# Kernel optimization log

Measured on AMD Instinct MI355X. Metric: run time of the kernel, lower is better.

## Reference

```python
import jax, jax.numpy as jnp
import numpy as np

NUM_FILTER = 256
CAPS_LEN = 8
NUM_EMOTIONS = 8
OUT_DIM = 16
NUM_CHANNEL = 25
TIME_LEN = 25
NUM_CAPS = NUM_CHANNEL * TIME_LEN * (NUM_FILTER // CAPS_LEN)  # 20000
NUM_ITERATIONS = 3


def setup_inputs() -> dict:
    key = jax.random.key(0)
    ks = jax.random.split(key, 10)
    B = 32
    x = jax.random.normal(ks[0], (B, 54, 54), jnp.float32)
    conv1_w = jax.random.normal(ks[1], (NUM_FILTER, 1, 6, 6), jnp.float32) * 0.05
    conv1_b = jax.random.normal(ks[2], (NUM_FILTER,), jnp.float32) * 0.01
    conv2_w = jax.random.normal(ks[3], (NUM_FILTER, NUM_FILTER, 6, 6), jnp.float32) * 0.01
    conv2_b = jax.random.normal(ks[4], (NUM_FILTER,), jnp.float32) * 0.01
    conv3_w = jax.random.normal(ks[5], (NUM_FILTER, 2 * NUM_FILTER, 1, 1), jnp.float32) * 0.05
    conv3_b = jax.random.normal(ks[6], (NUM_FILTER,), jnp.float32) * 0.01
    # PrimaryCaps: one Linear(caps_len -> caps_len) per capsule, batched as [nc, out, in]
    pc_w = jax.random.normal(ks[7], (NUM_CAPS, CAPS_LEN, CAPS_LEN), jnp.float32) * 0.1
    pc_b = jax.random.normal(ks[8], (NUM_CAPS, CAPS_LEN), jnp.float32) * 0.1
    # EmotionCaps transform W: [nc, num_emotions, out_dim, in_dim]
    W = jax.random.normal(ks[9], (NUM_CAPS, NUM_EMOTIONS, OUT_DIM, CAPS_LEN), jnp.float32) * 0.05
    return {"x": x, "conv1_w": conv1_w, "conv1_b": conv1_b, "conv2_w": conv2_w,
            "conv2_b": conv2_b, "conv3_w": conv3_w, "conv3_b": conv3_b,
            "pc_w": pc_w, "pc_b": pc_b, "W": W}


def _conv(x, w, b, stride):
    y = jax.lax.conv_general_dilated(x, w, (stride, stride), 'VALID',
                                     dimension_numbers=('NCHW', 'OIHW', 'NCHW'))
    return y + b[None, :, None, None]


def _squash(s):
    # scale = |s|^2 / (1 + |s|^2); out = scale * s / (|s| + 1e-8)
    n2 = jnp.sum(s * s, axis=-1, keepdims=True)
    n = jnp.sqrt(n2)
    return (n2 / (1.0 + n2)) * s / (n + 1e-8)


def reference(x, conv1_w, conv1_b, conv2_w, conv2_b, conv3_w, conv3_b, pc_w, pc_b, W):
    x4 = x[:, None]                                    # [B,1,54,54]
    x1 = jax.nn.relu(_conv(x4, conv1_w, conv1_b, 2))   # [B,F,25,25]
    y = jnp.pad(x1, ((0, 0), (0, 0), (2, 3), (2, 3)))  # ZeroPad2d((2,3,2,3))
    y = jax.nn.relu(_conv(y, conv2_w, conv2_b, 1))     # [B,F,25,25]
    z = jax.nn.relu(jnp.concatenate([x1, y], axis=1))  # [B,2F,25,25]
    z = _conv(z, conv3_w, conv3_b, 1)                  # [B,F,25,25]
    B, F, H, Wd = z.shape
    # flatten to capsules: [B, F//caps_len, caps_len, H*W] -> [B, nc, caps_len]
    caps = z.reshape(B, F // CAPS_LEN, CAPS_LEN, H * Wd)
    caps = caps.transpose(0, 1, 3, 2).reshape(B, NUM_CAPS, CAPS_LEN)
    # PrimaryCaps: per-capsule linear, batched as a single einsum
    u = jnp.einsum('bni,noi->bno', caps, pc_w) + pc_b[None]   # [B,nc,caps_len]
    # EmotionCaps: u_hat[b,n,e,o] = W[n,e,o,i] u[b,n,i]
    u_hat = jnp.einsum('bni,neoi->bneo', u, W)                # [B,nc,ne,out_dim]
    b = jnp.zeros((B, NUM_CAPS, NUM_EMOTIONS), u.dtype)
    v = None
    for r in range(NUM_ITERATIONS):
        c = jax.nn.softmax(b, axis=2)[..., None]              # [B,nc,ne,1]
        v = _squash(jnp.sum(c * u_hat, axis=1))               # [B,ne,out_dim]
        if r < NUM_ITERATIONS - 1:
            b = b + jnp.einsum('bneo,beo->bne', u_hat, v)
    return jnp.linalg.norm(v, axis=-1)                        # [B,ne]
```

## Files before the change

kernel.cpp:

```cpp
#include <hip/hip_runtime.h>
#include <hip/hip_fp16.h>

typedef unsigned short u16;
typedef __attribute__((ext_vector_type(8))) short bf16x8;
typedef __attribute__((ext_vector_type(4))) float floatx4;
typedef __attribute__((ext_vector_type(2))) _Float16 half2v;

#define NPIX 625
#define NCAPS 20000
#define K2 9216

__device__ __forceinline__ u16 f2bf(float f) {
  unsigned u = __float_as_uint(f);
  return (u16)((u + 0x7fffu + ((u >> 16) & 1u)) >> 16);
}

__device__ __forceinline__ unsigned h16(float f) {
  union { _Float16 h; u16 b; } c;
  c.h = (_Float16)f;
  return (unsigned)c.b;
}

__device__ __forceinline__ half2v as_h2(unsigned u) {
  union { unsigned i; half2v h; } c;
  c.i = u;
  return c.h;
}

__device__ __forceinline__ float dot2f(unsigned a, unsigned b, float c) {
#if __has_builtin(__builtin_amdgcn_fdot2)
  return __builtin_amdgcn_fdot2(as_h2(a), as_h2(b), c, false);
#else
  half2v x = as_h2(a), y = as_h2(b);
  return fmaf((float)x[1], (float)y[1], fmaf((float)x[0], (float)y[0], c));
#endif
}

__device__ __forceinline__ float dotrow16(uint4 w, uint4 u) {
  float s = dot2f(w.x, u.x, 0.f);
  s = dot2f(w.y, u.y, s);
  s = dot2f(w.z, u.z, s);
  s = dot2f(w.w, u.w, s);
  return s;
}

__device__ __forceinline__ float dot8v(float4 a0, float4 a1, float4 b0, float4 b1) {
  float s = a0.x * b0.x;
  s = fmaf(a0.y, b0.y, s); s = fmaf(a0.z, b0.z, s); s = fmaf(a0.w, b0.w, s);
  s = fmaf(a1.x, b1.x, s); s = fmaf(a1.y, b1.y, s);
  s = fmaf(a1.z, b1.z, s); s = fmaf(a1.w, b1.w, s);
  return s;
}

#define GLDS16(g, l) __builtin_amdgcn_global_load_lds( \
    (const __attribute__((address_space(1))) void*)(g), \
    (__attribute__((address_space(3))) void*)(l), 16, 0, 0)

__global__ void prep_conv1(const float* __restrict__ w2, const float* __restrict__ w3,
                           u16* __restrict__ A2c, u16* __restrict__ A3,
                           const float* __restrict__ x, const float* __restrict__ w1,
                           const float* __restrict__ b1, u16* __restrict__ x1p) {
  if (blockIdx.x < 256) {
    const int oc = blockIdx.x, c = threadIdx.x;
    const float* src = w2 + (oc * 256 + c) * 36;
    float v[36];
#pragma unroll
    for (int k = 0; k < 9; k++) {
      const float4 q = *(const float4*)(src + k * 4);
      v[k * 4 + 0] = q.x; v[k * 4 + 1] = q.y; v[k * 4 + 2] = q.z; v[k * 4 + 3] = q.w;
    }
    const int mtile = oc >> 7, row = oc & 127;
#pragma unroll
    for (int t = 0; t < 36; t++) {
      const int kt = t / 9, tl = t % 9;
      A2c[(kt * 2 + mtile) * 294912 + row * 2304 + tl * 256 + c] = f2bf(v[t]);
    }
  } else if (blockIdx.x < 384) {
    const int j = (blockIdx.x - 256) * 1024 + threadIdx.x * 4;
    const float4 q = *(const float4*)(w3 + j);
    ushort4 p;
    p.x = f2bf(q.x); p.y = f2bf(q.y); p.z = f2bf(q.z); p.w = f2bf(q.w);
    *(ushort4*)(A3 + j) = p;
  } else {
    const int blk = blockIdx.x - 384;
    const int b = blk / 25, i = blk % 25;
    const int f = threadIdx.x;
    float wreg[36];
#pragma unroll
    for (int k = 0; k < 36; k++) wreg[k] = w1[f * 36 + k];
    float bias = b1[f];
    const float* xb = x + b * 54 * 54 + (2 * i) * 54;
    for (int j = 0; j < 25; j++) {
      float acc = bias;
#pragma unroll
      for (int ki = 0; ki < 6; ki++)
#pragma unroll
        for (int kj = 0; kj < 6; kj++)
          acc = fmaf(xb[ki * 54 + 2 * j + kj], wreg[ki * 6 + kj], acc);
      x1p[(((b * 30 + i + 2) * 30) + (j + 2)) * 256 + f] = f2bf(fmaxf(acc, 0.f));
    }
  }
}

__global__ __launch_bounds__(256) void conv2_gemm(const u16* __restrict__ A2c,
    const u16* __restrict__ x1p, u16* __restrict__ P) {
  __shared__ u16 As0[128 * 32];
  __shared__ u16 Bs0[128 * 32];
  __shared__ u16 As1[128 * 32];
  __shared__ u16 Bs1[128 * 32];
  const int tid = threadIdx.x;
  const int lane = tid & 63, wave = tid >> 6;
  const int f = blockIdx.x;
  const int w = (f & 7) * 157 + (f >> 3);
  const int ntile = w >> 3, combo = w & 7;
  const int kt = combo >> 1, mtile = combo & 1;
  const int t0 = kt * 9;

  const int seg0 = tid, seg1 = tid + 256;
  const u16* gA0 = A2c + combo * 294912 + (seg0 >> 2) * 2304 + (seg0 & 3) * 8;
  const u16* gA1 = A2c + combo * 294912 + (seg1 >> 2) * 2304 + (seg1 & 3) * 8;

  auto pixbase = [&](int seg) {
    int n = ntile * 128 + (seg >> 2);
    if (n > NCAPS - 1) n = NCAPS - 1;
    int b = n / NPIX, p = n % NPIX;
    int i = p / 25, j = p % 25;
    return ((b * 30 + i) * 30 + j) * 256 + (seg & 3) * 8;
  };
  const u16* gb0 = x1p + pixbase(seg0);
  const u16* gb1 = x1p + pixbase(seg1);

  floatx4 acc[4][4] = {};
  const int wm = wave & 1, wn = wave >> 1;
  const int lrow = lane & 15, kgrp = lane >> 4;

  int kj = t0 % 6;
  int boff = ((t0 / 6) * 30 + kj) * 256;
  for (int t = 0; t < 9; t++) {
#pragma unroll 1
    for (int cc = 0; cc < 8; cc += 2) {
      const int b0 = boff + cc * 32;
      GLDS16(gA0, As0 + seg0 * 8);
      GLDS16(gA1, As0 + seg1 * 8);
      GLDS16(gA0 + 32, As1 + seg0 * 8);
      GLDS16(gA1 + 32, As1 + seg1 * 8);
      GLDS16(gb0 + b0, Bs0 + seg0 * 8);
      GLDS16(gb1 + b0, Bs0 + seg1 * 8);
      GLDS16(gb0 + b0 + 32, Bs1 + seg0 * 8);
      GLDS16(gb1 + b0 + 32, Bs1 + seg1 * 8);
      gA0 += 64; gA1 += 64;
      __syncthreads();
      bf16x8 af[4], bfr[4];
#pragma unroll
      for (int tt = 0; tt < 4; tt++) {
        af[tt]  = *(const bf16x8*)(As0 + (wm * 64 + tt * 16 + lrow) * 32 + kgrp * 8);
        bfr[tt] = *(const bf16x8*)(Bs0 + (wn * 64 + tt * 16 + lrow) * 32 + kgrp * 8);
      }
#pragma unroll
      for (int tm = 0; tm < 4; tm++)
#pragma unroll
        for (int tn = 0; tn < 4; tn++)
          acc[tm][tn] = __builtin_amdgcn_mfma_f32_16x16x32_bf16(af[tm], bfr[tn], acc[tm][tn], 0, 0, 0);
#pragma unroll
      for (int tt = 0; tt < 4; tt++) {
        af[tt]  = *(const bf16x8*)(As1 + (wm * 64 + tt * 16 + lrow) * 32 + kgrp * 8);
        bfr[tt] = *(const bf16x8*)(Bs1 + (wn * 64 + tt * 16 + lrow) * 32 + kgrp * 8);
      }
#pragma unroll
      for (int tm = 0; tm < 4; tm++)
#pragma unroll
        for (int tn = 0; tn < 4; tn++)
          acc[tm][tn] = __builtin_amdgcn_mfma_f32_16x16x32_bf16(af[tm], bfr[tn], acc[tm][tn], 0, 0, 0);
      __syncthreads();
    }
    boff += 256;
    kj++;
    if (kj == 6) { kj = 0; boff += 6144; }
  }

  u16* Pk = P + kt * 5120000;
  const int nb = ntile * 128 + wn * 64;
  const int ocb = mtile * 128 + wm * 64 + kgrp * 4;
#pragma unroll
  for (int tn = 0; tn < 4; tn++) {
    int n = nb + tn * 16 + lrow;
    if (n < NCAPS) {
#pragma unroll
      for (int tm = 0; tm < 4; tm++) {
        int oc = ocb + tm * 16;
        ushort4 pk;
        pk.x = f2bf(acc[tm][tn][0]);
        pk.y = f2bf(acc[tm][tn][1]);
        pk.z = f2bf(acc[tm][tn][2]);
        pk.w = f2bf(acc[tm][tn][3]);
        *(ushort4*)(Pk + n * 256 + oc) = pk;
      }
    }
  }
}

__global__ void conv2_red(const u16* __restrict__ P, const float* __restrict__ bias2,
                          u16* __restrict__ y) {
  const int idx = blockIdx.x * 256 + threadIdx.x;
  const ushort4 p0 = *(const ushort4*)(P + idx * 4);
  const ushort4 p1 = *(const ushort4*)(P + 5120000 + idx * 4);
  const ushort4 p2 = *(const ushort4*)(P + 10240000 + idx * 4);
  const ushort4 p3 = *(const ushort4*)(P + 15360000 + idx * 4);
  const float4 bs = *(const float4*)(bias2 + ((idx * 4) & 255));
  auto bf = [](unsigned v) { return __uint_as_float(v << 16); };
  float sx = bf(p0.x) + bf(p1.x) + bf(p2.x) + bf(p3.x) + bs.x;
  float sy = bf(p0.y) + bf(p1.y) + bf(p2.y) + bf(p3.y) + bs.y;
  float sz = bf(p0.z) + bf(p1.z) + bf(p2.z) + bf(p3.z) + bs.z;
  float sw = bf(p0.w) + bf(p1.w) + bf(p2.w) + bf(p3.w) + bs.w;
  ushort4 pk;
  pk.x = f2bf(fmaxf(sx, 0.f));
  pk.y = f2bf(fmaxf(sy, 0.f));
  pk.z = f2bf(fmaxf(sz, 0.f));
  pk.w = f2bf(fmaxf(sw, 0.f));
  *(ushort4*)(y + idx * 4) = pk;
}

__global__ __launch_bounds__(256) void conv3_gemm(const u16* __restrict__ A3,
    const u16* __restrict__ x1p, const u16* __restrict__ y, u16* __restrict__ P3) {
  __shared__ u16 As[128 * 32];
  __shared__ u16 Bs[128 * 32];
  const int tid = threadIdx.x;
  const int lane = tid & 63, wave = tid >> 6;
  const int mtile = blockIdx.x, ntile = blockIdx.y, kt = blockIdx.z;

  const int seg0 = tid, seg1 = tid + 256;
  const u16* ga0 = A3 + (mtile * 128 + (seg0 >> 2)) * 512 + (seg0 & 3) * 8 + kt * 256;
  const u16* ga1 = A3 + (mtile * 128 + (seg1 >> 2)) * 512 + (seg1 & 3) * 8 + kt * 256;

  auto mkbase = [&](int seg) {
    int n = ntile * 128 + (seg >> 2);
    if (n > NCAPS - 1) n = NCAPS - 1;
    if (kt == 0) {
      int b = n / NPIX, p = n % NPIX;
      int i = p / 25, j = p % 25;
      return x1p + ((b * 30 + i + 2) * 30 + (j + 2)) * 256 + (seg & 3) * 8;
    }
    return y + n * 256 + (seg & 3) * 8;
  };
  const u16* gs0 = mkbase(seg0);
  const u16* gs1 = mkbase(seg1);

  floatx4 acc[4][4] = {};
  const int wm = wave & 1, wn = wave >> 1;
  const int lrow = lane & 15, kgrp = lane >> 4;

  for (int kc = 0; kc < 8; kc++) {
    GLDS16(ga0 + kc * 32, As + seg0 * 8);
    GLDS16(ga1 + kc * 32, As + seg1 * 8);
    GLDS16(gs0 + kc * 32, Bs + seg0 * 8);
    GLDS16(gs1 + kc * 32, Bs + seg1 * 8);
    __syncthreads();
    bf16x8 af[4], bfr[4];
#pragma unroll
    for (int tt = 0; tt < 4; tt++) {
      af[tt]  = *(const bf16x8*)(As + (wm * 64 + tt * 16 + lrow) * 32 + kgrp * 8);
      bfr[tt] = *(const bf16x8*)(Bs + (wn * 64 + tt * 16 + lrow) * 32 + kgrp * 8);
    }
#pragma unroll
    for (int tm = 0; tm < 4; tm++)
#pragma unroll
      for (int tn = 0; tn < 4; tn++)
        acc[tm][tn] = __builtin_amdgcn_mfma_f32_16x16x32_bf16(af[tm], bfr[tn], acc[tm][tn], 0, 0, 0);
    __syncthreads();
  }

  u16* Pk = P3 + kt * 5120000;
  const int nb = ntile * 128 + wn * 64;
  const int fb = mtile * 128 + wm * 64 + kgrp * 4;
#pragma unroll
  for (int tn = 0; tn < 4; tn++) {
    int n = nb + tn * 16 + lrow;
    if (n < NCAPS) {
#pragma unroll
      for (int tm = 0; tm < 4; tm++) {
        int f0 = fb + tm * 16;
        ushort4 pk;
        pk.x = f2bf(acc[tm][tn][0]);
        pk.y = f2bf(acc[tm][tn][1]);
        pk.z = f2bf(acc[tm][tn][2]);
        pk.w = f2bf(acc[tm][tn][3]);
        *(ushort4*)(Pk + n * 256 + f0) = pk;
      }
    }
  }
}

__global__ void prep_caps(const float* __restrict__ W, u16* __restrict__ Wbs,
                          const u16* __restrict__ P3, const float* __restrict__ b3,
                          const float* __restrict__ pcw, const float* __restrict__ pcb,
                          unsigned* __restrict__ u2) {
  const int tid = threadIdx.x;
  if (blockIdx.x < 10000) {
    int r = blockIdx.x * 256 + tid;
    int n = r >> 7, eo = r & 127;
    int e = eo >> 4, o = eo & 15;
    const float* src = W + n * 1024 + eo * 8;
    const float4 v0 = *(const float4*)src;
    const float4 v1 = *(const float4*)(src + 4);
    u16* dst = Wbs + n * 1088 + e * 136 + o * 8;
    ushort4 p0, p1;
    p0.x = (u16)h16(v0.x); p0.y = (u16)h16(v0.y); p0.z = (u16)h16(v0.z); p0.w = (u16)h16(v0.w);
    p1.x = (u16)h16(v1.x); p1.y = (u16)h16(v1.y); p1.z = (u16)h16(v1.z); p1.w = (u16)h16(v1.w);
    *(ushort4*)dst = p0;
    *(ushort4*)(dst + 4) = p1;
  } else {
    const int blk = blockIdx.x - 10000;
    const int b = tid >> 3, o = tid & 7;
    for (int k = 0; k < 8; k++) {
      const int n = blk * 8 + k;
      const int g = n / NPIX, p = n % NPIX;
      const u16* pa = P3 + ((b * NPIX + p) * 256 + g * 8);
      const uint4 qa = *(const uint4*)pa;
      const uint4 qb = *(const uint4*)(pa + 5120000);
      const float* bp = b3 + g * 8;
      const float4 bb0 = *(const float4*)bp;
      const float4 bb1 = *(const float4*)(bp + 4);
      float4 c0, c1;
      c0.x = __uint_as_float(qa.x << 16) + __uint_as_float(qb.x << 16) + bb0.x;
      c0.y = __uint_as_float(qa.x & 0xffff0000u) + __uint_as_float(qb.x & 0xffff0000u) + bb0.y;
      c0.z = __uint_as_float(qa.y << 16) + __uint_as_float(qb.y << 16) + bb0.z;
      c0.w = __uint_as_float(qa.y & 0xffff0000u) + __uint_as_float(qb.y & 0xffff0000u) + bb0.w;
      c1.x = __uint_as_float(qa.z << 16) + __uint_as_float(qb.z << 16) + bb1.x;
      c1.y = __uint_as_float(qa.z & 0xffff0000u) + __uint_as_float(qb.z & 0xffff0000u) + bb1.y;
      c1.z = __uint_as_float(qa.w << 16) + __uint_as_float(qb.w << 16) + bb1.z;
      c1.w = __uint_as_float(qa.w & 0xffff0000u) + __uint_as_float(qb.w & 0xffff0000u) + bb1.w;
      const float* pw = pcw + n * 64 + o * 8;
      float4 w0 = *(const float4*)pw;
      float4 w1 = *(const float4*)(pw + 4);
      const float myu = pcb[n * 8 + o] + dot8v(w0, w1, c0, c1);
      const float partner = __shfl_xor(myu, 1, 64);
      if (!(o & 1)) {
        unsigned pk = h16(myu) | (h16(partner) << 16);
        u2[n * 128 + b * 4 + (o >> 1)] = pk;
      }
    }
  }
}

__global__ __launch_bounds__(256, 4) void caps_accb2(const unsigned* __restrict__ u2,
    const u16* __restrict__ Wbs, const float* __restrict__ vsum,
    float* __restrict__ Spart, int zero_v) {
  __shared__ u16 Ws[16 * 1088];
  const int tid = threadIdx.x;
  const int b = tid >> 3, e = tid & 7;
  const int n0 = blockIdx.x * 16;

  const u16* gsrc = Wbs + n0 * 1088;
#pragma unroll
  for (int k = 0; k < 9; k++) {
    const int idx = k * 256 + tid;
    if (idx < 2176) GLDS16(gsrc + idx * 8, Ws + idx * 8);
  }

  float4 V0 = make_float4(0.f, 0.f, 0.f, 0.f), V1 = V0, V2 = V0, V3 = V0;
  if (!zero_v) {
    const float* vp = vsum + tid * 16;
    V0 = *(const float4*)vp;
    V1 = *(const float4*)(vp + 4);
    V2 = *(const float4*)(vp + 8);
    V3 = *(const float4*)(vp + 12);
  }
  float s0 = 0.f, s1 = 0.f, s2 = 0.f, s3 = 0.f, s4 = 0.f, s5 = 0.f, s6 = 0.f, s7 = 0.f;
  float s8 = 0.f, s9 = 0.f, s10 = 0.f, s11 = 0.f, s12 = 0.f, s13 = 0.f, s14 = 0.f, s15 = 0.f;

  __syncthreads();

  for (int it = 0; it < 16; it++) {
    const int n = n0 + it;
    const uint4 up = *(const uint4*)(u2 + n * 128 + b * 4);
    const u16* Wn = Ws + it * 1088 + e * 136;
    float h0, h1, h2, h3, h4, h5, h6, h7, h8, h9, h10, h11, h12, h13, h14, h15;
#define ROW(o, H) { uint4 w = *(const uint4*)(Wn + (o) * 8); H = dotrow16(w, up); }
    ROW(0, h0)   ROW(1, h1)   ROW(2, h2)   ROW(3, h3)
    ROW(4, h4)   ROW(5, h5)   ROW(6, h6)   ROW(7, h7)
    ROW(8, h8)   ROW(9, h9)   ROW(10, h10) ROW(11, h11)
    ROW(12, h12) ROW(13, h13) ROW(14, h14) ROW(15, h15)
#undef ROW
    float c;
    if (zero_v) {
      c = 0.125f;
    } else {
      float blog = h0 * V0.x;
      blog = fmaf(h1, V0.y, blog);  blog = fmaf(h2, V0.z, blog);  blog = fmaf(h3, V0.w, blog);
      blog = fmaf(h4, V1.x, blog);  blog = fmaf(h5, V1.y, blog);  blog = fmaf(h6, V1.z, blog);
      blog = fmaf(h7, V1.w, blog);  blog = fmaf(h8, V2.x, blog);  blog = fmaf(h9, V2.y, blog);
      blog = fmaf(h10, V2.z, blog); blog = fmaf(h11, V2.w, blog); blog = fmaf(h12, V3.x, blog);
      blog = fmaf(h13, V3.y, blog); blog = fmaf(h14, V3.z, blog); blog = fmaf(h15, V3.w, blog);
      float m = blog;
      m = fmaxf(m, __shfl_xor(m, 1, 64));
      m = fmaxf(m, __shfl_xor(m, 2, 64));
      m = fmaxf(m, __shfl_xor(m, 4, 64));
      float ex = __expf(blog - m);
      float ss = ex;
      ss += __shfl_xor(ss, 1, 64);
      ss += __shfl_xor(ss, 2, 64);
      ss += __shfl_xor(ss, 4, 64);
      c = ex / ss;
    }
    s0 = fmaf(c, h0, s0);   s1 = fmaf(c, h1, s1);   s2 = fmaf(c, h2, s2);   s3 = fmaf(c, h3, s3);
    s4 = fmaf(c, h4, s4);   s5 = fmaf(c, h5, s5);   s6 = fmaf(c, h6, s6);   s7 = fmaf(c, h7, s7);
    s8 = fmaf(c, h8, s8);   s9 = fmaf(c, h9, s9);   s10 = fmaf(c, h10, s10); s11 = fmaf(c, h11, s11);
    s12 = fmaf(c, h12, s12); s13 = fmaf(c, h13, s13); s14 = fmaf(c, h14, s14); s15 = fmaf(c, h15, s15);
  }
  float* Sp = Spart + blockIdx.x * 4096 + tid * 16;
  *(float4*)(Sp + 0)  = make_float4(s0, s1, s2, s3);
  *(float4*)(Sp + 4)  = make_float4(s4, s5, s6, s7);
  *(float4*)(Sp + 8)  = make_float4(s8, s9, s10, s11);
  *(float4*)(Sp + 12) = make_float4(s12, s13, s14, s15);
}

__global__ void caps_redB(const float* __restrict__ Spart, float* __restrict__ Sp2) {
  const int j = blockIdx.x * 256 + threadIdx.x;
  const int r0 = blockIdx.y * 50;
  float a0 = 0.f, a1 = 0.f;
  for (int r = 0; r < 50; r += 2) {
    a0 += Spart[(r0 + r) * 4096 + j];
    a1 += Spart[(r0 + r + 1) * 4096 + j];
  }
  Sp2[blockIdx.y * 4096 + j] = a0 + a1;
}

__global__ void caps_v2(const float* __restrict__ Sp2, float* __restrict__ vsum, int add) {
  const int t = threadIdx.x;
  float4 a0 = make_float4(0.f, 0.f, 0.f, 0.f), a1 = a0, a2 = a0, a3 = a0;
  for (int r = 0; r < 25; r++) {
    const float* sp = Sp2 + r * 4096 + t * 16;
    const float4 q0 = *(const float4*)sp;
    const float4 q1 = *(const float4*)(sp + 4);
    const float4 q2 = *(const float4*)(sp + 8);
    const float4 q3 = *(const float4*)(sp + 12);
    a0.x += q0.x; a0.y += q0.y; a0.z += q0.z; a0.w += q0.w;
    a1.x += q1.x; a1.y += q1.y; a1.z += q1.z; a1.w += q1.w;
    a2.x += q2.x; a2.y += q2.y; a2.z += q2.z; a2.w += q2.w;
    a3.x += q3.x; a3.y += q3.y; a3.z += q3.z; a3.w += q3.w;
  }
  float n2 = a0.x * a0.x;
  n2 = fmaf(a0.y, a0.y, n2); n2 = fmaf(a0.z, a0.z, n2); n2 = fmaf(a0.w, a0.w, n2);
  n2 = fmaf(a1.x, a1.x, n2); n2 = fmaf(a1.y, a1.y, n2); n2 = fmaf(a1.z, a1.z, n2); n2 = fmaf(a1.w, a1.w, n2);
  n2 = fmaf(a2.x, a2.x, n2); n2 = fmaf(a2.y, a2.y, n2); n2 = fmaf(a2.z, a2.z, n2); n2 = fmaf(a2.w, a2.w, n2);
  n2 = fmaf(a3.x, a3.x, n2); n2 = fmaf(a3.y, a3.y, n2); n2 = fmaf(a3.z, a3.z, n2); n2 = fmaf(a3.w, a3.w, n2);
  const float n = sqrtf(n2);
  const float scale = n2 / ((1.f + n2) * (n + 1e-8f));
  float* vp = vsum + t * 16;
  float4 o0, o1, o2, o3;
  if (add) {
    o0 = *(float4*)(vp + 0); o1 = *(float4*)(vp + 4); o2 = *(float4*)(vp + 8); o3 = *(float4*)(vp + 12);
  } else {
    o0 = make_float4(0.f, 0.f, 0.f, 0.f); o1 = o0; o2 = o0; o3 = o0;
  }
  o0.x = fmaf(a0.x, scale, o0.x); o0.y = fmaf(a0.y, scale, o0.y);
  o0.z = fmaf(a0.z, scale, o0.z); o0.w = fmaf(a0.w, scale, o0.w);
  o1.x = fmaf(a1.x, scale, o1.x); o1.y = fmaf(a1.y, scale, o1.y);
  o1.z = fmaf(a1.z, scale, o1.z); o1.w = fmaf(a1.w, scale, o1.w);
  o2.x = fmaf(a2.x, scale, o2.x); o2.y = fmaf(a2.y, scale, o2.y);
  o2.z = fmaf(a2.z, scale, o2.z); o2.w = fmaf(a2.w, scale, o2.w);
  o3.x = fmaf(a3.x, scale, o3.x); o3.y = fmaf(a3.y, scale, o3.y);
  o3.z = fmaf(a3.z, scale, o3.z); o3.w = fmaf(a3.w, scale, o3.w);
  *(float4*)(vp + 0) = o0; *(float4*)(vp + 4) = o1;
  *(float4*)(vp + 8) = o2; *(float4*)(vp + 12) = o3;
}

__global__ void caps_out2(const float* __restrict__ Sp2, float* __restrict__ out) {
  const int t = threadIdx.x;
  float4 a0 = make_float4(0.f, 0.f, 0.f, 0.f), a1 = a0, a2 = a0, a3 = a0;
  for (int r = 0; r < 25; r++) {
    const float* sp = Sp2 + r * 4096 + t * 16;
    const float4 q0 = *(const float4*)sp;
    const float4 q1 = *(const float4*)(sp + 4);
    const float4 q2 = *(const float4*)(sp + 8);
    const float4 q3 = *(const float4*)(sp + 12);
    a0.x += q0.x; a0.y += q0.y; a0.z += q0.z; a0.w += q0.w;
    a1.x += q1.x; a1.y += q1.y; a1.z += q1.z; a1.w += q1.w;
    a2.x += q2.x; a2.y += q2.y; a2.z += q2.z; a2.w += q2.w;
    a3.x += q3.x; a3.y += q3.y; a3.z += q3.z; a3.w += q3.w;
  }
  float n2 = a0.x * a0.x;
  n2 = fmaf(a0.y, a0.y, n2); n2 = fmaf(a0.z, a0.z, n2); n2 = fmaf(a0.w, a0.w, n2);
  n2 = fmaf(a1.x, a1.x, n2); n2 = fmaf(a1.y, a1.y, n2); n2 = fmaf(a1.z, a1.z, n2); n2 = fmaf(a1.w, a1.w, n2);
  n2 = fmaf(a2.x, a2.x, n2); n2 = fmaf(a2.y, a2.y, n2); n2 = fmaf(a2.z, a2.z, n2); n2 = fmaf(a2.w, a2.w, n2);
  n2 = fmaf(a3.x, a3.x, n2); n2 = fmaf(a3.y, a3.y, n2); n2 = fmaf(a3.z, a3.z, n2); n2 = fmaf(a3.w, a3.w, n2);
  const float n = sqrtf(n2);
  out[t] = n * n2 / ((1.f + n2) * (n + 1e-8f));
}

extern "C" void kernel_launch(void* const* d_in, const int* in_sizes, int n_in,
                              void* d_out, int out_size, void* d_ws, size_t ws_size,
                              hipStream_t stream) {
  const float* x   = (const float*)d_in[0];
  const float* w1  = (const float*)d_in[1];
  const float* b1  = (const float*)d_in[2];
  const float* w2  = (const float*)d_in[3];
  const float* b2  = (const float*)d_in[4];
  const float* w3  = (const float*)d_in[5];
  const float* b3  = (const float*)d_in[6];
  const float* pcw = (const float*)d_in[7];
  const float* pcb = (const float*)d_in[8];
  const float* W   = (const float*)d_in[9];
  float* out = (float*)d_out;

  char* ws = (char*)d_ws;

  u16*   x1p = (u16*)(ws + 0);
  u16*   A2  = (u16*)(ws + 14745600);
  u16*   A3  = (u16*)(ws + 19464192);
  u16*   y   = (u16*)(ws + 19726336);
  u16*   P   = (u16*)(ws + 29966336);
  u16*   P3  = (u16*)(ws + 43520000);
  u16*   Wbs = (u16*)(ws + 0);
  float* Spart = (float*)(ws + 43520000);
  unsigned* u2 = (unsigned*)(ws + 64000000);
  float* Sp2 = (float*)(ws + 74240000);
  float* vs  = (float*)(ws + 74649600);

  hipMemsetAsync(x1p, 0, 14745600, stream);

  prep_conv1<<<1184, 256, 0, stream>>>(w2, w3, A2, A3, x, w1, b1, x1p);
  conv2_gemm<<<1256, 256, 0, stream>>>(A2, x1p, P);
  conv2_red<<<5000, 256, 0, stream>>>(P, b2, y);
  conv3_gemm<<<dim3(2, 157, 2), 256, 0, stream>>>(A3, x1p, y, P3);
  prep_caps<<<12500, 256, 0, stream>>>(W, Wbs, P3, b3, pcw, pcb, u2);

  for (int pass = 0; pass < 3; pass++) {
    caps_accb2<<<1250, 256, 0, stream>>>(u2, Wbs, vs, Spart, pass == 0 ? 1 : 0);
    caps_redB<<<dim3(16, 25), 256, 0, stream>>>(Spart, Sp2);
    if (pass == 0)      caps_v2<<<1, 256, 0, stream>>>(Sp2, vs, 0);
    else if (pass == 1) caps_v2<<<1, 256, 0, stream>>>(Sp2, vs, 1);
    else                caps_out2<<<1, 256, 0, stream>>>(Sp2, out);
  }
}
```

Measured before the change: 442.5 us.

## Retile conv2 GEMM to 256x160 blocks with double-buffered swizzled LDS

New measurement: 454.0 us. +2.6%, slower.

```diff
diff --git a/kernel.cpp b/kernel.cpp
--- a/kernel.cpp
+++ b/kernel.cpp
@@ -69,11 +69,10 @@
       const float4 q = *(const float4*)(src + k * 4);
       v[k * 4 + 0] = q.x; v[k * 4 + 1] = q.y; v[k * 4 + 2] = q.z; v[k * 4 + 3] = q.w;
     }
-    const int mtile = oc >> 7, row = oc & 127;
-#pragma unroll
-    for (int t = 0; t < 36; t++) {
-      const int kt = t / 9, tl = t % 9;
-      A2c[(kt * 2 + mtile) * 294912 + row * 2304 + tl * 256 + c] = f2bf(v[t]);
+#pragma unroll
+    for (int g = 0; g < 36; g++) {
+      const int ktp = g / 9, tl = g % 9;
+      A2c[(ktp * 256 + oc) * 2304 + tl * 256 + c] = f2bf(v[g]);
     }
   } else if (blockIdx.x < 384) {
     const int j = (blockIdx.x - 256) * 1024 + threadIdx.x * 4;
@@ -102,99 +101,104 @@
   }
 }
 
-__global__ __launch_bounds__(256) void conv2_gemm(const u16* __restrict__ A2c,
+__global__ __launch_bounds__(512, 2) void conv2_gemm(const u16* __restrict__ A2n,
     const u16* __restrict__ x1p, u16* __restrict__ P) {
-  __shared__ u16 As0[128 * 32];
-  __shared__ u16 Bs0[128 * 32];
-  __shared__ u16 As1[128 * 32];
-  __shared__ u16 Bs1[128 * 32];
+  __shared__ __align__(16) u16 lds[2][26624];
   const int tid = threadIdx.x;
   const int lane = tid & 63, wave = tid >> 6;
-  const int f = blockIdx.x;
-  const int w = (f & 7) * 157 + (f >> 3);
-  const int ntile = w >> 3, combo = w & 7;
-  const int kt = combo >> 1, mtile = combo & 1;
-  const int t0 = kt * 9;
-
-  const int seg0 = tid, seg1 = tid + 256;
-  const u16* gA0 = A2c + combo * 294912 + (seg0 >> 2) * 2304 + (seg0 & 3) * 8;
-  const u16* gA1 = A2c + combo * 294912 + (seg1 >> 2) * 2304 + (seg1 & 3) * 8;
-
-  auto pixbase = [&](int seg) {
-    int n = ntile * 128 + (seg >> 2);
-    if (n > NCAPS - 1) n = NCAPS - 1;
-    int b = n / NPIX, p = n % NPIX;
-    int i = p / 25, j = p % 25;
-    return ((b * 30 + i) * 30 + j) * 256 + (seg & 3) * 8;
+  const int ntile = blockIdx.x, kt = blockIdx.y;
+  const int wm = wave & 3, wn = wave >> 2;
+  const int lrow = lane & 15, kg = lane >> 4;
+  const bool extra = (tid < 256);
+
+  const int trow = tid >> 3;
+  const int xoff = 8 * ((tid & 7) ^ (trow & 7));
+  const u16* aSrc = A2n + (kt * 256 + trow) * 2304 + xoff;
+  const int nb = ntile * 160;
+  auto pixrow = [&](int r) {
+    const int n = nb + r;
+    const int b = n / NPIX, p = n % NPIX;
+    const int i = p / 25, j = p % 25;
+    return ((b * 30 + i) * 30 + j) * 256;
   };
-  const u16* gb0 = x1p + pixbase(seg0);
-  const u16* gb1 = x1p + pixbase(seg1);
-
-  floatx4 acc[4][4] = {};
-  const int wm = wave & 1, wn = wave >> 1;
-  const int lrow = lane & 15, kgrp = lane >> 4;
-
-  int kj = t0 % 6;
-  int boff = ((t0 / 6) * 30 + kj) * 256;
-  for (int t = 0; t < 9; t++) {
-#pragma unroll 1
-    for (int cc = 0; cc < 8; cc += 2) {
-      const int b0 = boff + cc * 32;
-      GLDS16(gA0, As0 + seg0 * 8);
-      GLDS16(gA1, As0 + seg1 * 8);
-      GLDS16(gA0 + 32, As1 + seg0 * 8);
-      GLDS16(gA1 + 32, As1 + seg1 * 8);
-      GLDS16(gb0 + b0, Bs0 + seg0 * 8);
-      GLDS16(gb1 + b0, Bs0 + seg1 * 8);
-      GLDS16(gb0 + b0 + 32, Bs1 + seg0 * 8);
-      GLDS16(gb1 + b0 + 32, Bs1 + seg1 * 8);
-      gA0 += 64; gA1 += 64;
-      __syncthreads();
-      bf16x8 af[4], bfr[4];
-#pragma unroll
-      for (int tt = 0; tt < 4; tt++) {
-        af[tt]  = *(const bf16x8*)(As0 + (wm * 64 + tt * 16 + lrow) * 32 + kgrp * 8);
-        bfr[tt] = *(const bf16x8*)(Bs0 + (wn * 64 + tt * 16 + lrow) * 32 + kgrp * 8);
-      }
-#pragma unroll
-      for (int tm = 0; tm < 4; tm++)
-#pragma unroll
-        for (int tn = 0; tn < 4; tn++)
-          acc[tm][tn] = __builtin_amdgcn_mfma_f32_16x16x32_bf16(af[tm], bfr[tn], acc[tm][tn], 0, 0, 0);
-#pragma unroll
-      for (int tt = 0; tt < 4; tt++) {
-        af[tt]  = *(const bf16x8*)(As1 + (wm * 64 + tt * 16 + lrow) * 32 + kgrp * 8);
-        bfr[tt] = *(const bf16x8*)(Bs1 + (wn * 64 + tt * 16 + lrow) * 32 + kgrp * 8);
-      }
-#pragma unroll
-      for (int tm = 0; tm < 4; tm++)
-#pragma unroll
-        for (int tn = 0; tn < 4; tn++)
-          acc[tm][tn] = __builtin_amdgcn_mfma_f32_16x16x32_bf16(af[tm], bfr[tn], acc[tm][tn], 0, 0, 0);
-      __syncthreads();
-    }
-    boff += 256;
-    kj++;
-    if (kj == 6) { kj = 0; boff += 6144; }
+  const u16* bSrc0 = x1p + pixrow(trow) + xoff;
+  const u16* bSrc1 = x1p + pixrow(64 + trow) + xoff;
+  const u16* bSrc2 = extra ? (x1p + pixrow(128 + trow) + xoff) : x1p;
+
+  auto stage = [&](int bb, int t) {
+    u16* Ab = &lds[bb][0];
+    u16* Bb = &lds[bb][16384];
+    const int g = kt * 9 + (t >> 2);
+    const int boff = ((g / 6) * 30 + (g % 6)) * 256 + (t & 3) * 64;
+    const u16* a = aSrc + t * 64;
+#pragma unroll
+    for (int i = 0; i < 4; i++)
+      GLDS16(a + i * (64 * 2304), Ab + i * 4096 + tid * 8);
+    GLDS16(bSrc0 + boff, Bb + tid * 8);
+    GLDS16(bSrc1 + boff, Bb + 4096 + tid * 8);
+    if (extra) GLDS16(bSrc2 + boff, Bb + 8192 + tid * 8);
+  };
+
+  floatx4 acc[4][5] = {};
+  const int jx0 = 8 * (kg ^ (lrow & 7));
+  const int jx1 = 8 * ((4 + kg) ^ (lrow & 7));
+  const int arow = wm * 64 + lrow;
+  const int brow = wn * 80 + lrow;
+
+  stage(0, 0);
+  for (int t = 0; t < 36; t++) {
+    const int bb = t & 1;
+    if (t < 35) {
+      stage(bb ^ 1, t + 1);
+      if (extra) asm volatile("s_waitcnt vmcnt(7)" ::: "memory");
+      else       asm volatile("s_waitcnt vmcnt(6)" ::: "memory");
+    } else {
+      asm volatile("s_waitcnt vmcnt(0)" ::: "memory");
+    }
+    __builtin_amdgcn_s_barrier();
+    asm volatile("" ::: "memory");
+    const u16* Ab = &lds[bb][0];
+    const u16* Bb = &lds[bb][16384];
+    bf16x8 af0[4], b0[5], af1[4], b1r[5];
+#pragma unroll
+    for (int fm = 0; fm < 4; fm++) af0[fm] = *(const bf16x8*)(Ab + (arow + fm * 16) * 64 + jx0);
+#pragma unroll
+    for (int fn = 0; fn < 5; fn++) b0[fn] = *(const bf16x8*)(Bb + (brow + fn * 16) * 64 + jx0);
+    __builtin_amdgcn_s_setprio(1);
+#pragma unroll
+    for (int fm = 0; fm < 4; fm++)
+#pragma unroll
+      for (int fn = 0; fn < 5; fn++)
+        acc[fm][fn] = __builtin_amdgcn_mfma_f32_16x16x32_bf16(af0[fm], b0[fn], acc[fm][fn], 0, 0, 0);
+    __builtin_amdgcn_s_setprio(0);
+#pragma unroll
+    for (int fm = 0; fm < 4; fm++) af1[fm] = *(const bf16x8*)(Ab + (arow + fm * 16) * 64 + jx1);
+#pragma unroll
+    for (int fn = 0; fn < 5; fn++) b1r[fn] = *(const bf16x8*)(Bb + (brow + fn * 16) * 64 + jx1);
+    __builtin_amdgcn_s_setprio(1);
+#pragma unroll
+    for (int fm = 0; fm < 4; fm++)
+#pragma unroll
+      for (int fn = 0; fn < 5; fn++)
+        acc[fm][fn] = __builtin_amdgcn_mfma_f32_16x16x32_bf16(af1[fm], b1r[fn], acc[fm][fn], 0, 0, 0);
+    __builtin_amdgcn_s_setprio(0);
+    asm volatile("" ::: "memory");
+    __builtin_amdgcn_s_barrier();
   }
 
   u16* Pk = P + kt * 5120000;
-  const int nb = ntile * 128 + wn * 64;
-  const int ocb = mtile * 128 + wm * 64 + kgrp * 4;
-#pragma unroll
-  for (int tn = 0; tn < 4; tn++) {
-    int n = nb + tn * 16 + lrow;
-    if (n < NCAPS) {
-#pragma unroll
-      for (int tm = 0; tm < 4; tm++) {
-        int oc = ocb + tm * 16;
-        ushort4 pk;
-        pk.x = f2bf(acc[tm][tn][0]);
-        pk.y = f2bf(acc[tm][tn][1]);
-        pk.z = f2bf(acc[tm][tn][2]);
-        pk.w = f2bf(acc[tm][tn][3]);
-        *(ushort4*)(Pk + n * 256 + oc) = pk;
-      }
+#pragma unroll
+  for (int fn = 0; fn < 5; fn++) {
+    const int n = nb + wn * 80 + fn * 16 + lrow;
+#pragma unroll
+    for (int fm = 0; fm < 4; fm++) {
+      const int oc = wm * 64 + fm * 16 + kg * 4;
+      ushort4 pk;
+      pk.x = f2bf(acc[fm][fn][0]);
+      pk.y = f2bf(acc[fm][fn][1]);
+      pk.z = f2bf(acc[fm][fn][2]);
+      pk.w = f2bf(acc[fm][fn][3]);
+      *(ushort4*)(Pk + n * 256 + oc) = pk;
     }
   }
 }
@@ -520,7 +524,7 @@
   hipMemsetAsync(x1p, 0, 14745600, stream);
 
   prep_conv1<<<1184, 256, 0, stream>>>(w2, w3, A2, A3, x, w1, b1, x1p);
-  conv2_gemm<<<1256, 256, 0, stream>>>(A2, x1p, P);
+  conv2_gemm<<<dim3(125, 4), 512, 0, stream>>>(A2, x1p, P);
   conv2_red<<<5000, 256, 0, stream>>>(P, b2, y);
   conv3_gemm<<<dim3(2, 157, 2), 256, 0, stream>>>(A3, x1p, y, P3);
   prep_caps<<<12500, 256, 0, stream>>>(W, Wbs, P3, b3, pcw, pcb, u2);
```
